# Optimization experiments

Measured on AMD Instinct MI355X. Metric: run time of the kernel, lower is better.

The kernel has to match this reference:

```python
import jax, jax.numpy as jnp
import numpy as np

N_INPUT, N_HIDDEN, N_OUTPUT = 64, 1024, 64
B, T = 128, 512

def setup_inputs() -> dict:
    key = jax.random.key(0)
    ks = jax.random.split(key, 8)
    s_in = 1.0 / np.sqrt(N_INPUT)
    s_h = 1.0 / np.sqrt(N_HIDDEN)
    return {
        "x": jax.random.normal(ks[0], (B, T, N_INPUT), jnp.float32),
        "enc_w": jax.random.uniform(ks[1], (N_HIDDEN, N_INPUT), jnp.float32, -s_in, s_in),
        "enc_b": jax.random.uniform(ks[2], (N_HIDDEN,), jnp.float32, -s_in, s_in),
        "rec_w": jax.random.uniform(ks[3], (N_HIDDEN, N_HIDDEN), jnp.float32, -s_h, s_h),
        "fgt_w": jax.random.uniform(ks[4], (N_HIDDEN, N_HIDDEN), jnp.float32, -s_h, s_h),
        "dec_w": jax.random.uniform(ks[5], (N_OUTPUT, N_HIDDEN), jnp.float32, -s_h, s_h),
        "dec_b": jax.random.uniform(ks[6], (N_OUTPUT,), jnp.float32, -s_h, s_h),
        "hinit_w": jax.random.uniform(ks[7], (N_HIDDEN, 1), jnp.float32, -1.0, 1.0),
        "hinit_b": jax.random.uniform(jax.random.fold_in(key, 9), (N_HIDDEN,), jnp.float32, -1.0, 1.0),
    }

def softsign(x):
    return x / (1.0 + jnp.abs(x))

def reference(x, enc_w, enc_b, rec_w, fgt_w, dec_w, dec_b, hinit_w, hinit_b):
    # x: [B, T, I] -> time-major [T, B, I]
    xt = jnp.transpose(x, (1, 0, 2))
    # hidden_init(ones(B,1)) = ones @ hinit_w^T + b = broadcast of column sum
    hidden0 = jnp.broadcast_to(hinit_w[:, 0] + hinit_b, (x.shape[0], hinit_b.shape[0]))
    # Precompute encoder projection for all timesteps (same math, one big GEMM)
    enc_all = jnp.einsum('tbi,hi->tbh', xt, enc_w) + enc_b  # [T, B, H]

    def step(hidden, enc_t):
        forget = jax.nn.sigmoid(hidden @ fgt_w.T)
        hidden_new = softsign(enc_t + hidden @ rec_w.T)
        hidden = (1.0 - forget) * hidden + forget * hidden_new
        out_t = hidden @ dec_w.T + dec_b
        return hidden, out_t

    hidden, output = jax.lax.scan(step, hidden0, enc_all)
    return output, hidden  # output: [T, B, O], hidden: [B, H]
```

## Files before the change

### kernel.cpp

```cpp
#include <hip/hip_runtime.h>

typedef unsigned short u16;

#define NWG 256
#define NT  256
#define TS  512
#define HD  1024
#define BS  128
#define NI  64
#define NO  64
#define XR  16
#define CC  32
#define RCP 17

typedef __attribute__((ext_vector_type(8))) short bf16x8;
typedef __attribute__((ext_vector_type(4))) float f32x4;

__device__ __forceinline__ float bf2f(u16 u) {
    union { unsigned int i; float f; } v; v.i = ((unsigned int)u) << 16; return v.f;
}
__device__ __forceinline__ u16 f2bf(float f) {
    union { float fl; unsigned int i; } v; v.fl = f;
    unsigned int x = v.i;
    return (u16)((x + 0x7fffu + ((x >> 16) & 1u)) >> 16);
}
__device__ __forceinline__ float ldv(const void* p, size_t i, bool isf32) {
    return isf32 ? ((const float*)p)[i] : bf2f(((const u16*)p)[i]);
}

__device__ __forceinline__ unsigned l2_atomic_add(unsigned* p, unsigned v) {
    unsigned old;
    asm volatile("global_atomic_add %0, %1, %2, off sc0\n\t"
                 "s_waitcnt vmcnt(0)"
                 : "=&v"(old) : "v"(p), "v"(v) : "memory");
    return old;
}

__device__ __forceinline__ void load_a_frags(const u16* ap, bf16x8* a) {
    asm volatile(
        "global_load_dwordx4 %0, %8, off sc0\n\t"
        "global_load_dwordx4 %1, %8, off offset:64 sc0\n\t"
        "global_load_dwordx4 %2, %8, off offset:128 sc0\n\t"
        "global_load_dwordx4 %3, %8, off offset:192 sc0\n\t"
        "global_load_dwordx4 %4, %8, off offset:256 sc0\n\t"
        "global_load_dwordx4 %5, %8, off offset:320 sc0\n\t"
        "global_load_dwordx4 %6, %8, off offset:384 sc0\n\t"
        "global_load_dwordx4 %7, %8, off offset:448 sc0\n\t"
        "s_waitcnt vmcnt(0)"
        : "=&v"(a[0]), "=&v"(a[1]), "=&v"(a[2]), "=&v"(a[3]),
          "=&v"(a[4]), "=&v"(a[5]), "=&v"(a[6]), "=&v"(a[7])
        : "v"(ap) : "memory");
}

#define CNT_STRIDE 16

__global__ __launch_bounds__(NT)
void arnn_xcd(const void* __restrict__ xv,
              const void* __restrict__ encwv,
              const void* __restrict__ encbv,
              const void* __restrict__ recwv,
              const void* __restrict__ fgtwv,
              const void* __restrict__ decwv,
              const void* __restrict__ decbv,
              const void* __restrict__ hinitwv,
              const void* __restrict__ hinitbv,
              void* __restrict__ outv,
              u16* __restrict__ h0buf,
              u16* __restrict__ h1buf,
              unsigned* __restrict__ tickets,
              unsigned* __restrict__ cnts)
{
    __shared__ short WB[132 * 64 * 8];
    __shared__ float redC[4 * 5 * 16 * RCP];
    __shared__ float hst[XR * CC];
    __shared__ float encbS[CC];
    __shared__ float decbLS[16];
    __shared__ unsigned s_xcd, s_slot;
    __shared__ int s_f32;

    const int tid  = threadIdx.x;
    const int wave = tid >> 6;
    const int lane = tid & 63;
    const int m    = lane & 15;
    const int quad = lane >> 4;

    if (tid == 0) {
        unsigned xcc;
        asm volatile("s_getreg_b32 %0, hwreg(HW_REG_XCC_ID, 0, 4)" : "=s"(xcc));
        xcc &= 7u;
        unsigned slot = l2_atomic_add(tickets + xcc * 16, 1u);
        s_xcd = xcc;
        s_slot = slot & 31u;
        s_f32 = 0;
    }
    __syncthreads();
    {
        float v = bf2f(((const u16*)recwv)[tid]);
        if (!(v >= -1.0f && v <= 1.0f)) s_f32 = 1;
    }
    __syncthreads();
    const bool isf32 = (s_f32 != 0);
    const int xcd  = (int)s_xcd;
    const int slot = (int)s_slot;
    const int b0   = xcd * XR;
    const int j0   = slot * CC;
    const int dt   = slot & 3;
    unsigned* qcnt = cnts + (size_t)xcd * 520 * CNT_STRIDE;

    for (int idx = tid; idx < 132 * 64; idx += NT) {
        int ksg = idx >> 6, l = idx & 63, n = l & 15, q = l >> 4;
        int tile, ksl;
        if (ksg < 34)       { tile = 0; ksl = ksg; }
        else if (ksg < 68)  { tile = 1; ksl = ksg - 34; }
        else if (ksg < 100) { tile = 2; ksl = ksg - 68; }
        else                { tile = 3; ksl = ksg - 100; }
        int j = j0 + ((tile & 1) << 4) + n;
        bf16x8 v;
        if (!isf32) {
            const u16* src;
            if (tile < 2) src = (ksl < 32) ? (const u16*)recwv + (size_t)j * HD + ksl * 32 + q * 8
                                           : (const u16*)encwv + (size_t)j * NI + (ksl - 32) * 32 + q * 8;
            else          src = (const u16*)fgtwv + (size_t)j * HD + ksl * 32 + q * 8;
            v = *(const bf16x8*)src;
        } else {
            const float* src;
            if (tile < 2) src = (ksl < 32) ? (const float*)recwv + (size_t)j * HD + ksl * 32 + q * 8
                                           : (const float*)encwv + (size_t)j * NI + (ksl - 32) * 32 + q * 8;
            else          src = (const float*)fgtwv + (size_t)j * HD + ksl * 32 + q * 8;
            #pragma unroll
            for (int i = 0; i < 8; ++i) v[i] = (short)f2bf(src[i]);
        }
        *(bf16x8*)&WB[idx * 8] = v;
    }

    bf16x8 dfr[8];
    {
        int o = 16 * dt + m;
        #pragma unroll
        for (int ks = 0; ks < 8; ++ks) {
            int kb = wave * 256 + ks * 32 + quad * 8;
            if (!isf32) dfr[ks] = *(const bf16x8*)((const u16*)decwv + (size_t)o * HD + kb);
            else {
                const float* src = (const float*)decwv + (size_t)o * HD + kb;
                #pragma unroll
                for (int i = 0; i < 8; ++i) dfr[ks][i] = (short)f2bf(src[i]);
            }
        }
    }
    if (tid < CC) encbS[tid] = ldv(encbv, j0 + tid, isf32);
    if (tid < 16) decbLS[tid] = ldv(decbv, 16 * dt + tid, isf32);
    for (int e = tid; e < XR * CC; e += NT) {
        int r = e >> 5, c = e & 31;
        float v = ldv(hinitwv, j0 + c, isf32) + ldv(hinitbv, j0 + c, isf32);
        hst[e] = v;
        h0buf[(size_t)(b0 + r) * HD + j0 + c] = f2bf(v);
    }
    __syncthreads();
    if (tid == 0) l2_atomic_add(qcnt + 0 * CNT_STRIDE, 1u);

    for (int t = 0; t < TS; ++t) {
        if (wave == 0) {
            if (lane == 0) {
                unsigned* p = qcnt + (size_t)t * CNT_STRIDE;
                while (l2_atomic_add(p, 0u) < 32u) __builtin_amdgcn_s_sleep(2);
            }
        }
        __syncthreads();

        const u16* cur = (t & 1) ? h1buf : h0buf;
        u16*       nxt = (t & 1) ? h0buf : h1buf;

        bf16x8 a[8];
        load_a_frags(cur + (size_t)(b0 + m) * HD + wave * 256 + quad * 8, a);

        bf16x8 xf;
        if (wave < 2) {
            size_t xb = (size_t)(b0 + m) * (TS * NI) + (size_t)t * NI + wave * 32 + quad * 8;
            if (!isf32) xf = *(const bf16x8*)((const u16*)xv + xb);
            else {
                const float* xp = (const float*)xv + xb;
                #pragma unroll
                for (int i = 0; i < 8; ++i) xf[i] = (short)f2bf(xp[i]);
            }
        }

        f32x4 acc[5];
        #pragma unroll
        for (int tt = 0; tt < 5; ++tt) acc[tt] = (f32x4){0.f, 0.f, 0.f, 0.f};

        #pragma unroll
        for (int ks = 0; ks < 8; ++ks) {
            int kb = wave * 8 + ks;
            bf16x8 bf0 = *(const bf16x8*)&WB[((0   + kb) * 64 + lane) * 8];
            bf16x8 bf1 = *(const bf16x8*)&WB[((34  + kb) * 64 + lane) * 8];
            bf16x8 bf2 = *(const bf16x8*)&WB[((68  + kb) * 64 + lane) * 8];
            bf16x8 bf3 = *(const bf16x8*)&WB[((100 + kb) * 64 + lane) * 8];
            acc[0] = __builtin_amdgcn_mfma_f32_16x16x32_bf16(a[ks], bf0, acc[0], 0, 0, 0);
            acc[1] = __builtin_amdgcn_mfma_f32_16x16x32_bf16(a[ks], bf1, acc[1], 0, 0, 0);
            acc[2] = __builtin_amdgcn_mfma_f32_16x16x32_bf16(a[ks], bf2, acc[2], 0, 0, 0);
            acc[3] = __builtin_amdgcn_mfma_f32_16x16x32_bf16(a[ks], bf3, acc[3], 0, 0, 0);
            acc[4] = __builtin_amdgcn_mfma_f32_16x16x32_bf16(a[ks], dfr[ks], acc[4], 0, 0, 0);
        }
        if (wave < 2) {
            bf16x8 e0 = *(const bf16x8*)&WB[((32 + wave) * 64 + lane) * 8];
            bf16x8 e1 = *(const bf16x8*)&WB[((34 + 32 + wave) * 64 + lane) * 8];
            acc[0] = __builtin_amdgcn_mfma_f32_16x16x32_bf16(xf, e0, acc[0], 0, 0, 0);
            acc[1] = __builtin_amdgcn_mfma_f32_16x16x32_bf16(xf, e1, acc[1], 0, 0, 0);
        }

        #pragma unroll
        for (int tt = 0; tt < 5; ++tt) {
            #pragma unroll
            for (int r = 0; r < 4; ++r)
                redC[((wave * 5 + tt) * 16 + quad * 4 + r) * RCP + m] = acc[tt][r];
        }
        __syncthreads();

        for (int e = tid; e < XR * CC; e += NT) {
            int r = e >> 5, c = e & 31, tl = c >> 4, col = c & 15;
            float pr = encbS[c], pf = 0.f;
            #pragma unroll
            for (int kq = 0; kq < 4; ++kq) {
                pr += redC[((kq * 5 + tl) * 16 + r) * RCP + col];
                pf += redC[((kq * 5 + 2 + tl) * 16 + r) * RCP + col];
            }
            float fg = 1.0f / (1.0f + __expf(-pf));
            float hn = pr / (1.0f + fabsf(pr));
            float h  = hst[e];
            float hv = h + fg * (hn - h);
            hst[e] = hv;
            nxt[(size_t)(b0 + r) * HD + j0 + c] = f2bf(hv);
        }
        __syncthreads();
        if (tid == 0) l2_atomic_add(qcnt + (size_t)(t + 1) * CNT_STRIDE, 1u);

        if (slot < 4 && t > 0) {
            int r = tid >> 4, col = tid & 15;
            float o = decbLS[col];
            #pragma unroll
            for (int kq = 0; kq < 4; ++kq)
                o += redC[((kq * 5 + 4) * 16 + r) * RCP + col];
            size_t oi = (size_t)(t - 1) * (BS * NO) + (size_t)(b0 + r) * NO + 16 * dt + col;
            if (isf32) ((float*)outv)[oi] = o; else ((u16*)outv)[oi] = f2bf(o);
        }
    }

    if (wave == 0) {
        if (lane == 0) {
            unsigned* p = qcnt + (size_t)TS * CNT_STRIDE;
            while (l2_atomic_add(p, 0u) < 32u) __builtin_amdgcn_s_sleep(2);
        }
    }
    __syncthreads();
    {
        bf16x8 a[8];
        load_a_frags(h0buf + (size_t)(b0 + m) * HD + wave * 256 + quad * 8, a);
        f32x4 ac = (f32x4){0.f, 0.f, 0.f, 0.f};
        #pragma unroll
        for (int ks = 0; ks < 8; ++ks)
            ac = __builtin_amdgcn_mfma_f32_16x16x32_bf16(a[ks], dfr[ks], ac, 0, 0, 0);
        #pragma unroll
        for (int r = 0; r < 4; ++r)
            redC[((wave * 5 + 4) * 16 + quad * 4 + r) * RCP + m] = ac[r];
        __syncthreads();
        if (slot < 4) {
            int r = tid >> 4, col = tid & 15;
            float o = decbLS[col];
            #pragma unroll
            for (int kq = 0; kq < 4; ++kq)
                o += redC[((kq * 5 + 4) * 16 + r) * RCP + col];
            size_t oi = (size_t)511 * (BS * NO) + (size_t)(b0 + r) * NO + 16 * dt + col;
            if (isf32) ((float*)outv)[oi] = o; else ((u16*)outv)[oi] = f2bf(o);
        }
        for (int e = tid; e < XR * CC; e += NT) {
            int r = e >> 5, c = e & 31;
            size_t oi = (size_t)TS * BS * NO + (size_t)(b0 + r) * HD + j0 + c;
            float v = hst[e];
            if (isf32) ((float*)outv)[oi] = v; else ((u16*)outv)[oi] = f2bf(v);
        }
    }
}

extern "C" void kernel_launch(void* const* d_in, const int* in_sizes, int n_in,
                              void* d_out, int out_size, void* d_ws, size_t ws_size,
                              hipStream_t stream) {
    (void)in_sizes; (void)n_in; (void)out_size; (void)ws_size;
    const void* xv       = d_in[0];
    const void* encwv    = d_in[1];
    const void* encbv    = d_in[2];
    const void* recwv    = d_in[3];
    const void* fgtwv    = d_in[4];
    const void* decwv    = d_in[5];
    const void* decbv    = d_in[6];
    const void* hinitwv  = d_in[7];
    const void* hinitbv  = d_in[8];
    void* outv = d_out;

    unsigned* tickets = (unsigned*)d_ws;
    unsigned* cnts    = (unsigned*)((char*)d_ws + 4096);
    u16* h0buf = (u16*)((char*)d_ws + 524288);
    u16* h1buf = h0buf + (size_t)BS * HD;

    hipMemsetAsync(d_ws, 0, 4096 + 8 * 520 * 64, stream);

    void* args[] = { (void*)&xv, (void*)&encwv, (void*)&encbv, (void*)&recwv,
                     (void*)&fgtwv, (void*)&decwv, (void*)&decbv,
                     (void*)&hinitwv, (void*)&hinitbv,
                     (void*)&outv, (void*)&h0buf, (void*)&h1buf,
                     (void*)&tickets, (void*)&cnts };
    hipLaunchCooperativeKernel((void*)arnn_xcd, dim3(NWG), dim3(NT), args, 0, stream);
}
```

Before: 1.756 ms.

## Cache half of recurrent weights in registers and overlap input MFMA with barrier wait

Two of the four recurrent/forget weight fragment sets and the encoder weight fragments are preloaded from LDS into registers once, before the time loop, which removes per-step LDS reads for them. The input-projection MFMAs now run before the grid-wide spin-wait, so they overlap the wait for the previous step's hidden state. The spin sleep interval is shortened, and a non-cooperative launch fallback is added. The extra resident registers (16 more bf16x8 fragments) raise register pressure and may cause spills or lower occupancy.

```diff
diff --git a/kernel.cpp b/kernel.cpp
--- a/kernel.cpp
+++ b/kernel.cpp
@@ -132,7 +132,20 @@
         }
         *(bf16x8*)&WB[idx * 8] = v;
     }
-
+    __syncthreads();
+
+    bf16x8 Breg[2][8];
+    #pragma unroll
+    for (int ks = 0; ks < 8; ++ks) {
+        int kb = wave * 8 + ks;
+        Breg[0][ks] = *(const bf16x8*)&WB[((0  + kb) * 64 + lane) * 8];
+        Breg[1][ks] = *(const bf16x8*)&WB[((34 + kb) * 64 + lane) * 8];
+    }
+    bf16x8 Ereg[2];
+    if (wave < 2) {
+        Ereg[0] = *(const bf16x8*)&WB[((32 + wave) * 64 + lane) * 8];
+        Ereg[1] = *(const bf16x8*)&WB[((34 + 32 + wave) * 64 + lane) * 8];
+    }
     bf16x8 dfr[8];
     {
         int o = 16 * dt + m;
@@ -159,22 +172,12 @@
     if (tid == 0) l2_atomic_add(qcnt + 0 * CNT_STRIDE, 1u);
 
     for (int t = 0; t < TS; ++t) {
-        if (wave == 0) {
-            if (lane == 0) {
-                unsigned* p = qcnt + (size_t)t * CNT_STRIDE;
-                while (l2_atomic_add(p, 0u) < 32u) __builtin_amdgcn_s_sleep(2);
-            }
-        }
-        __syncthreads();
-
-        const u16* cur = (t & 1) ? h1buf : h0buf;
-        u16*       nxt = (t & 1) ? h0buf : h1buf;
-
-        bf16x8 a[8];
-        load_a_frags(cur + (size_t)(b0 + m) * HD + wave * 256 + quad * 8, a);
-
-        bf16x8 xf;
+        f32x4 acc[5];
+        #pragma unroll
+        for (int tt = 0; tt < 5; ++tt) acc[tt] = (f32x4){0.f, 0.f, 0.f, 0.f};
+
         if (wave < 2) {
+            bf16x8 xf;
             size_t xb = (size_t)(b0 + m) * (TS * NI) + (size_t)t * NI + wave * 32 + quad * 8;
             if (!isf32) xf = *(const bf16x8*)((const u16*)xv + xb);
             else {
@@ -182,30 +185,32 @@
                 #pragma unroll
                 for (int i = 0; i < 8; ++i) xf[i] = (short)f2bf(xp[i]);
             }
-        }
-
-        f32x4 acc[5];
-        #pragma unroll
-        for (int tt = 0; tt < 5; ++tt) acc[tt] = (f32x4){0.f, 0.f, 0.f, 0.f};
+            acc[0] = __builtin_amdgcn_mfma_f32_16x16x32_bf16(xf, Ereg[0], acc[0], 0, 0, 0);
+            acc[1] = __builtin_amdgcn_mfma_f32_16x16x32_bf16(xf, Ereg[1], acc[1], 0, 0, 0);
+        }
+
+        if (wave == 0 && lane == 0) {
+            unsigned* p = qcnt + (size_t)t * CNT_STRIDE;
+            while (l2_atomic_add(p, 0u) < 32u) __builtin_amdgcn_s_sleep(1);
+        }
+        __syncthreads();
+
+        const u16* cur = (t & 1) ? h1buf : h0buf;
+        u16*       nxt = (t & 1) ? h0buf : h1buf;
+
+        bf16x8 a[8];
+        load_a_frags(cur + (size_t)(b0 + m) * HD + wave * 256 + quad * 8, a);
 
         #pragma unroll
         for (int ks = 0; ks < 8; ++ks) {
             int kb = wave * 8 + ks;
-            bf16x8 bf0 = *(const bf16x8*)&WB[((0   + kb) * 64 + lane) * 8];
-            bf16x8 bf1 = *(const bf16x8*)&WB[((34  + kb) * 64 + lane) * 8];
             bf16x8 bf2 = *(const bf16x8*)&WB[((68  + kb) * 64 + lane) * 8];
             bf16x8 bf3 = *(const bf16x8*)&WB[((100 + kb) * 64 + lane) * 8];
-            acc[0] = __builtin_amdgcn_mfma_f32_16x16x32_bf16(a[ks], bf0, acc[0], 0, 0, 0);
-            acc[1] = __builtin_amdgcn_mfma_f32_16x16x32_bf16(a[ks], bf1, acc[1], 0, 0, 0);
-            acc[2] = __builtin_amdgcn_mfma_f32_16x16x32_bf16(a[ks], bf2, acc[2], 0, 0, 0);
-            acc[3] = __builtin_amdgcn_mfma_f32_16x16x32_bf16(a[ks], bf3, acc[3], 0, 0, 0);
-            acc[4] = __builtin_amdgcn_mfma_f32_16x16x32_bf16(a[ks], dfr[ks], acc[4], 0, 0, 0);
-        }
-        if (wave < 2) {
-            bf16x8 e0 = *(const bf16x8*)&WB[((32 + wave) * 64 + lane) * 8];
-            bf16x8 e1 = *(const bf16x8*)&WB[((34 + 32 + wave) * 64 + lane) * 8];
-            acc[0] = __builtin_amdgcn_mfma_f32_16x16x32_bf16(xf, e0, acc[0], 0, 0, 0);
-            acc[1] = __builtin_amdgcn_mfma_f32_16x16x32_bf16(xf, e1, acc[1], 0, 0, 0);
+            acc[0] = __builtin_amdgcn_mfma_f32_16x16x32_bf16(a[ks], Breg[0][ks], acc[0], 0, 0, 0);
+            acc[1] = __builtin_amdgcn_mfma_f32_16x16x32_bf16(a[ks], Breg[1][ks], acc[1], 0, 0, 0);
+            acc[2] = __builtin_amdgcn_mfma_f32_16x16x32_bf16(a[ks], bf2,         acc[2], 0, 0, 0);
+            acc[3] = __builtin_amdgcn_mfma_f32_16x16x32_bf16(a[ks], bf3,         acc[3], 0, 0, 0);
+            acc[4] = __builtin_amdgcn_mfma_f32_16x16x32_bf16(a[ks], dfr[ks],     acc[4], 0, 0, 0);
         }
 
         #pragma unroll
@@ -245,11 +250,9 @@
         }
     }
 
-    if (wave == 0) {
-        if (lane == 0) {
-            unsigned* p = qcnt + (size_t)TS * CNT_STRIDE;
-            while (l2_atomic_add(p, 0u) < 32u) __builtin_amdgcn_s_sleep(2);
-        }
+    if (wave == 0 && lane == 0) {
+        unsigned* p = qcnt + (size_t)TS * CNT_STRIDE;
+        while (l2_atomic_add(p, 0u) < 32u) __builtin_amdgcn_s_sleep(1);
     }
     __syncthreads();
     {
@@ -308,5 +311,10 @@
                      (void*)&hinitwv, (void*)&hinitbv,
                      (void*)&outv, (void*)&h0buf, (void*)&h1buf,
                      (void*)&tickets, (void*)&cnts };
-    hipLaunchCooperativeKernel((void*)arnn_xcd, dim3(NWG), dim3(NT), args, 0, stream);
-}
+    hipError_t err = hipLaunchCooperativeKernel((void*)arnn_xcd, dim3(NWG), dim3(NT), args, 0, stream);
+    if (err != hipSuccess) {
+        hipLaunchKernelGGL(arnn_xcd, dim3(NWG), dim3(NT), 0, stream,
+                           xv, encwv, encbv, recwv, fgtwv, decwv, decbv,
+                           hinitwv, hinitbv, outv, h0buf, h1buf, tickets, cnts);
+    }
+}
```

After: 1.627 ms. 7.3% less time.
